# Performance work log

Measured on AMD Instinct MI355X. Metric: run time of the kernel, lower is better.

The kernel has to match this reference:

```python
import jax, jax.numpy as jnp
import numpy as np

HID = 128   # hidden_dim
NCLS = 10   # n_classes
B = 64      # number of graphs in the batched heterograph
NC, NP, NN = 100000, 400000, 150000  # component / port / net node counts
E = 400000  # edges per edge type


def setup_inputs() -> dict:
    key = jax.random.key(0)
    ks = jax.random.split(key, 32)
    f32 = jnp.float32

    def w(k, shape, fan_in):
        return jax.random.normal(k, shape, dtype=f32) * (1.0 / np.sqrt(fan_in))

    inp = {
        "h_comp": jax.random.normal(ks[0], (NC, 1), f32),
        "h_port": jax.random.normal(ks[1], (NP, 2), f32),
        "h_net": jax.random.normal(ks[2], (NN, 1), f32),
        "e_cp_src": jax.random.randint(ks[3], (E,), 0, NC, dtype=jnp.int32),
        "e_cp_dst": jax.random.randint(ks[4], (E,), 0, NP, dtype=jnp.int32),
        "e_pn_src": jax.random.randint(ks[5], (E,), 0, NP, dtype=jnp.int32),
        "e_pn_dst": jax.random.randint(ks[6], (E,), 0, NN, dtype=jnp.int32),
        "gid_comp": jnp.sort(jax.random.randint(ks[7], (NC,), 0, B, dtype=jnp.int32)),
        "gid_port": jnp.sort(jax.random.randint(ks[8], (NP,), 0, B, dtype=jnp.int32)),
        "gid_net": jnp.sort(jax.random.randint(ks[9], (NN,), 0, B, dtype=jnp.int32)),
        # GraphConv weights/biases per (layer, edge_type)
        "W1_cp": w(ks[10], (1, HID), 1), "b1_cp": jnp.zeros((HID,), f32),
        "W1_pn": w(ks[11], (2, HID), 2), "b1_pn": jnp.zeros((HID,), f32),
        "W2_cp": w(ks[12], (HID, HID), HID), "b2_cp": jnp.zeros((HID,), f32),
        "W2_pn": w(ks[13], (HID, HID), HID), "b2_pn": jnp.zeros((HID,), f32),
        "W3_cp": w(ks[14], (HID, HID), HID), "b3_cp": jnp.zeros((HID,), f32),
        "W3_pn": w(ks[15], (HID, HID), HID), "b3_pn": jnp.zeros((HID,), f32),
        # classify MLP (input dim 4 = 1+2+1 pooled original features)
        "Wc1": w(ks[16], (4, HID), 4), "bc1": jnp.zeros((HID,), f32),
        "Wc2": w(ks[17], (HID, HID), HID), "bc2": jnp.zeros((HID,), f32),
        "Wc3": w(ks[18], (HID, NCLS), HID), "bc3": jnp.zeros((NCLS,), f32),
    }
    return inp


def reference(h_comp, h_port, h_net,
              e_cp_src, e_cp_dst, e_pn_src, e_pn_dst,
              gid_comp, gid_port, gid_net,
              W1_cp, b1_cp, W1_pn, b1_pn,
              W2_cp, b2_cp, W2_pn, b2_pn,
              W3_cp, b3_cp, W3_pn, b3_pn,
              Wc1, bc1, Wc2, bc2, Wc3, bc3):
    seg = jax.ops.segment_sum

    # --- HeteroGraphConv layers (faithful to original forward, including its
    # bug: DGL HeteroGraphConv drops node types with no incoming relation, so
    # 'component' vanishes after conv1 and 'port' after conv2; conv3 runs on an
    # empty dict; conv outputs are never written back to g, hence dead code).
    # GraphConv(norm='none'): dst = sum_{edges} (x_src @ W) + b
    port1 = jax.nn.relu(seg((h_comp @ W1_cp)[e_cp_src], e_cp_dst, num_segments=NP) + b1_cp)
    net1 = jax.nn.relu(seg((h_port @ W1_pn)[e_pn_src], e_pn_dst, num_segments=NN) + b1_pn)
    net2 = jax.nn.relu(seg((port1 @ W2_pn)[e_pn_src], e_pn_dst, num_segments=NN) + b2_pn)
    # conv3: skipped entirely (no src types remain in the feature dict)
    del net1, net2  # never used by the original module's output path

    # --- dgl.mean_nodes reads g.nodes[*].data['h'] = ORIGINAL input features
    def gmean(x, gid):
        s = seg(x, gid, num_segments=B)
        c = seg(jnp.ones((x.shape[0], 1), x.dtype), gid, num_segments=B)
        return s / jnp.maximum(c, 1.0)

    hg = jnp.concatenate([gmean(h_comp, gid_comp),
                          gmean(h_port, gid_port),
                          gmean(h_net, gid_net)], axis=1)  # [B, 4]

    h = jax.nn.relu(hg @ Wc1 + bc1)
    h = jax.nn.relu(h @ Wc2 + bc2)
    return h @ Wc3 + bc3  # [B, n_classes]
```

## Files before the change

kernel.cpp:

```cpp
#include <hip/hip_runtime.h>
#include <hip/hip_bf16.h>


#define NGRAPH 64
#define NB_COMP 120
#define NB_PORT 723
#define NB_NET  181
#define NSLOT (NB_COMP + NB_PORT + NB_NET)


template <int NF>
__device__ void reduce_type(const float* __restrict__ h, const int* __restrict__ gid, int n,
                            float (*bins)[NGRAPH][4],
                            int nblocks, int bid) {
    int nv = (n + 3) >> 2;
    int per = (nv + nblocks - 1) / nblocks;
    int start = bid * per;
    int end = min(nv, start + per);
    int set = threadIdx.x & 3;

    int cur = -1;
    float s0 = 0.f, s1 = 0.f, cnt = 0.f;

    for (int iv = start + (int)threadIdx.x; iv < end; iv += (int)blockDim.x) {
        int i = iv * 4;
        int g[4];
        float v0[4], v1[4];
        if (i + 3 < n) {
            int4 g4 = ((const int4*)gid)[iv];
            g[0] = g4.x; g[1] = g4.y; g[2] = g4.z; g[3] = g4.w;
            if (NF == 1) {
                float4 hv = ((const float4*)h)[iv];
                v0[0] = hv.x; v0[1] = hv.y; v0[2] = hv.z; v0[3] = hv.w;
            } else {
                float4 ha = ((const float4*)h)[iv * 2];
                float4 hb = ((const float4*)h)[iv * 2 + 1];
                v0[0] = ha.x; v1[0] = ha.y; v0[1] = ha.z; v1[1] = ha.w;
                v0[2] = hb.x; v1[2] = hb.y; v0[3] = hb.z; v1[3] = hb.w;
            }
        } else {
#pragma unroll
            for (int t = 0; t < 4; ++t) {
                if (i + t < n) {
                    g[t] = gid[i + t];
                    if (NF == 1) { v0[t] = h[i + t]; }
                    else { v0[t] = h[(i + t) * 2]; v1[t] = h[(i + t) * 2 + 1]; }
                } else {
                    g[t] = -2;
                    v0[t] = 0.f; v1[t] = 0.f;
                }
            }
        }
#pragma unroll
        for (int t = 0; t < 4; ++t) {
            if (g[t] == -2) continue;
            if (g[t] != cur) {
                if (cur >= 0) {
                    atomicAdd(&bins[set][cur][0], s0);
                    if (NF == 2) atomicAdd(&bins[set][cur][1], s1);
                    atomicAdd(&bins[set][cur][2], cnt);
                }
                cur = g[t]; s0 = 0.f; s1 = 0.f; cnt = 0.f;
            }
            s0 += v0[t];
            if (NF == 2) s1 += v1[t];
            cnt += 1.f;
        }
    }
    if (cur >= 0) {
        atomicAdd(&bins[set][cur][0], s0);
        if (NF == 2) atomicAdd(&bins[set][cur][1], s1);
        atomicAdd(&bins[set][cur][2], cnt);
    }
}

__global__ __launch_bounds__(256) void reduce_kernel(
    const float* __restrict__ h_comp, const float* __restrict__ h_port,
    const float* __restrict__ h_net,
    const int* __restrict__ gid_comp, const int* __restrict__ gid_port,
    const int* __restrict__ gid_net,
    int n_comp, int n_port, int n_net,
    float4* __restrict__ ws4) {
    __shared__ float bins[4][NGRAPH][4];
    int tid = threadIdx.x;
    int bid = blockIdx.x;

    for (int i = tid; i < 4 * NGRAPH * 4; i += blockDim.x) ((float*)bins)[i] = 0.f;
    __syncthreads();

    if (bid < NB_COMP) {
        reduce_type<1>(h_comp, gid_comp, n_comp, bins, NB_COMP, bid);
    } else if (bid < NB_COMP + NB_PORT) {
        reduce_type<2>(h_port, gid_port, n_port, bins, NB_PORT, bid - NB_COMP);
    } else {
        reduce_type<1>(h_net, gid_net, n_net, bins, NB_NET, bid - NB_COMP - NB_PORT);
    }
    __syncthreads();

    if (tid < NGRAPH) {
        float s0 = bins[0][tid][0] + bins[1][tid][0] + bins[2][tid][0] + bins[3][tid][0];
        float s1 = bins[0][tid][1] + bins[1][tid][1] + bins[2][tid][1] + bins[3][tid][1];
        float c  = bins[0][tid][2] + bins[1][tid][2] + bins[2][tid][2] + bins[3][tid][2];
        ws4[(size_t)tid * NSLOT + bid] = make_float4(s0, s1, c, 0.f);
    }
}

__global__ __launch_bounds__(256) void mlp_kernel(
    const float4* __restrict__ ws4,
    const float* __restrict__ Wc1, const float* __restrict__ bc1,
    const float* __restrict__ Wc2, const float* __restrict__ bc2,
    const float* __restrict__ Wc3, const float* __restrict__ bc3,
    float* __restrict__ out) {
    __shared__ float wred[4][8];
    __shared__ float hgs[4];
    __shared__ float h1[128];
    __shared__ float part[2][128];
    __shared__ float h2[128];
    __shared__ float l3[16][12];

    int g = blockIdx.x;
    int tid = threadIdx.x;

    float cs = 0.f, cc = 0.f, p0 = 0.f, p1 = 0.f, pc = 0.f, ns = 0.f, nc = 0.f;
    for (int s = tid; s < NSLOT; s += 256) {
        float4 v = ws4[(size_t)g * NSLOT + s];
        if (s < NB_COMP) { cs += v.x; cc += v.z; }
        else if (s < NB_COMP + NB_PORT) { p0 += v.x; p1 += v.y; pc += v.z; }
        else { ns += v.x; nc += v.z; }
    }
#pragma unroll
    for (int off = 32; off > 0; off >>= 1) {
        cs += __shfl_down(cs, off); cc += __shfl_down(cc, off);
        p0 += __shfl_down(p0, off); p1 += __shfl_down(p1, off);
        pc += __shfl_down(pc, off); ns += __shfl_down(ns, off);
        nc += __shfl_down(nc, off);
    }
    int wave = tid >> 6;
    if ((tid & 63) == 0) {
        wred[wave][0] = cs; wred[wave][1] = cc; wred[wave][2] = p0; wred[wave][3] = p1;
        wred[wave][4] = pc; wred[wave][5] = ns; wred[wave][6] = nc;
    }
    __syncthreads();
    if (tid == 0) {
        float t0 = wred[0][0] + wred[1][0] + wred[2][0] + wred[3][0];
        float t1 = wred[0][1] + wred[1][1] + wred[2][1] + wred[3][1];
        float t2 = wred[0][2] + wred[1][2] + wred[2][2] + wred[3][2];
        float t3 = wred[0][3] + wred[1][3] + wred[2][3] + wred[3][3];
        float t4 = wred[0][4] + wred[1][4] + wred[2][4] + wred[3][4];
        float t5 = wred[0][5] + wred[1][5] + wred[2][5] + wred[3][5];
        float t6 = wred[0][6] + wred[1][6] + wred[2][6] + wred[3][6];
        hgs[0] = t0 / fmaxf(t1, 1.f);
        hgs[1] = t2 / fmaxf(t4, 1.f);
        hgs[2] = t3 / fmaxf(t4, 1.f);
        hgs[3] = t5 / fmaxf(t6, 1.f);
    }
    __syncthreads();

    if (tid < 128) {
        float v = hgs[0] * Wc1[tid] + hgs[1] * Wc1[128 + tid] +
                  hgs[2] * Wc1[256 + tid] + hgs[3] * Wc1[384 + tid] + bc1[tid];
        h1[tid] = fmaxf(v, 0.f);
    }
    __syncthreads();

    {
        int j = tid & 127;
        int h = tid >> 7;
        float acc = 0.f;
#pragma unroll
        for (int kk = 0; kk < 64; kk += 4) {
            int k = h * 64 + kk;
            float4 hh = *(const float4*)&h1[k];
            acc += hh.x * Wc2[(k + 0) * 128 + j] + hh.y * Wc2[(k + 1) * 128 + j] +
                   hh.z * Wc2[(k + 2) * 128 + j] + hh.w * Wc2[(k + 3) * 128 + j];
        }
        part[h][j] = acc;
    }
    __syncthreads();
    if (tid < 128) h2[tid] = fmaxf(part[0][tid] + part[1][tid] + bc2[tid], 0.f);
    __syncthreads();

    if (tid < 160) {
        int c = tid % 10;
        int seg = tid / 10;
        float a = 0.f;
#pragma unroll
        for (int k = seg * 8; k < seg * 8 + 8; ++k) a += h2[k] * Wc3[k * 10 + c];
        l3[seg][c] = a;
    }
    __syncthreads();
    if (tid < 10) {
        float a = bc3[tid];
#pragma unroll
        for (int s = 0; s < 16; ++s) a += l3[s][tid];
        out[g * 10 + tid] = a;
    }
}

extern "C" void kernel_launch(void* const* d_in, const int* in_sizes, int n_in,
                              void* d_out, int out_size, void* d_ws, size_t ws_size,
                              hipStream_t stream) {
    const float* h_comp = (const float*)d_in[0];
    const float* h_port = (const float*)d_in[1];
    const float* h_net  = (const float*)d_in[2];
    const int* gid_comp = (const int*)d_in[7];
    const int* gid_port = (const int*)d_in[8];
    const int* gid_net  = (const int*)d_in[9];
    const float* Wc1 = (const float*)d_in[22];
    const float* bc1 = (const float*)d_in[23];
    const float* Wc2 = (const float*)d_in[24];
    const float* bc2 = (const float*)d_in[25];
    const float* Wc3 = (const float*)d_in[26];
    const float* bc3 = (const float*)d_in[27];

    int n_comp = in_sizes[0];
    int n_port = in_sizes[1] / 2;
    int n_net  = in_sizes[2];

    float4* ws4 = (float4*)d_ws;
    float* out = (float*)d_out;

    reduce_kernel<<<NSLOT, 256, 0, stream>>>(
        h_comp, h_port, h_net, gid_comp, gid_port, gid_net,
        n_comp, n_port, n_net, ws4);

    mlp_kernel<<<NGRAPH, 256, 0, stream>>>(ws4, Wc1, bc1, Wc2, bc2, Wc3, bc3, out);
}
```

Measured before the change: 117.7 us.

## Fuse reduce and MLP kernels into one cooperative launch with grid sync

Merges the per-graph reduction and the classifier MLP into a single cooperative kernel, separated by a grid-wide barrier, so only one launch is issued. The first 64 blocks run the MLP after the barrier. This removes the second launch and its gap. In exchange it adds grid-sync overhead, and cooperative launch requires all 1024 blocks to be co-resident. It falls back to the two-kernel path if the cooperative launch fails.

```diff
diff --git a/kernel.cpp b/kernel.cpp
--- a/kernel.cpp
+++ b/kernel.cpp
@@ -1,5 +1,8 @@
 #include <hip/hip_runtime.h>
 #include <hip/hip_bf16.h>
+#include <hip/hip_cooperative_groups.h>
+
+namespace cg = cooperative_groups;
 
 
 #define NGRAPH 64
@@ -74,6 +77,151 @@
     }
 }
 
+__device__ __forceinline__ void phase1(
+    const float* __restrict__ h_comp, const float* __restrict__ h_port,
+    const float* __restrict__ h_net,
+    const int* __restrict__ gid_comp, const int* __restrict__ gid_port,
+    const int* __restrict__ gid_net,
+    int n_comp, int n_port, int n_net,
+    float4* __restrict__ ws4, float (*bins)[NGRAPH][4]) {
+    int tid = threadIdx.x;
+    int bid = blockIdx.x;
+
+    for (int i = tid; i < 4 * NGRAPH * 4; i += 256) ((float*)bins)[i] = 0.f;
+    __syncthreads();
+
+    if (bid < NB_COMP) {
+        reduce_type<1>(h_comp, gid_comp, n_comp, bins, NB_COMP, bid);
+    } else if (bid < NB_COMP + NB_PORT) {
+        reduce_type<2>(h_port, gid_port, n_port, bins, NB_PORT, bid - NB_COMP);
+    } else {
+        reduce_type<1>(h_net, gid_net, n_net, bins, NB_NET, bid - NB_COMP - NB_PORT);
+    }
+    __syncthreads();
+
+    if (tid < NGRAPH) {
+        float s0 = bins[0][tid][0] + bins[1][tid][0] + bins[2][tid][0] + bins[3][tid][0];
+        float s1 = bins[0][tid][1] + bins[1][tid][1] + bins[2][tid][1] + bins[3][tid][1];
+        float c  = bins[0][tid][2] + bins[1][tid][2] + bins[2][tid][2] + bins[3][tid][2];
+        ws4[(size_t)tid * NSLOT + bid] = make_float4(s0, s1, c, 0.f);
+    }
+}
+
+__device__ __forceinline__ void phase2(
+    int g, const float4* __restrict__ ws4,
+    const float* __restrict__ Wc1, const float* __restrict__ bc1,
+    const float* __restrict__ Wc2, const float* __restrict__ bc2,
+    const float* __restrict__ Wc3, const float* __restrict__ bc3,
+    float* __restrict__ out,
+    float (*wred)[8], float* hgs, float* h1, float (*part)[128],
+    float* h2, float (*l3)[12]) {
+    int tid = threadIdx.x;
+
+    float cs = 0.f, cc = 0.f, p0 = 0.f, p1 = 0.f, pc = 0.f, ns = 0.f, nc = 0.f;
+    for (int s = tid; s < NSLOT; s += 256) {
+        float4 v = ws4[(size_t)g * NSLOT + s];
+        if (s < NB_COMP) { cs += v.x; cc += v.z; }
+        else if (s < NB_COMP + NB_PORT) { p0 += v.x; p1 += v.y; pc += v.z; }
+        else { ns += v.x; nc += v.z; }
+    }
+#pragma unroll
+    for (int off = 32; off > 0; off >>= 1) {
+        cs += __shfl_down(cs, off); cc += __shfl_down(cc, off);
+        p0 += __shfl_down(p0, off); p1 += __shfl_down(p1, off);
+        pc += __shfl_down(pc, off); ns += __shfl_down(ns, off);
+        nc += __shfl_down(nc, off);
+    }
+    int wave = tid >> 6;
+    if ((tid & 63) == 0) {
+        wred[wave][0] = cs; wred[wave][1] = cc; wred[wave][2] = p0; wred[wave][3] = p1;
+        wred[wave][4] = pc; wred[wave][5] = ns; wred[wave][6] = nc;
+    }
+    __syncthreads();
+    if (tid == 0) {
+        float t0 = wred[0][0] + wred[1][0] + wred[2][0] + wred[3][0];
+        float t1 = wred[0][1] + wred[1][1] + wred[2][1] + wred[3][1];
+        float t2 = wred[0][2] + wred[1][2] + wred[2][2] + wred[3][2];
+        float t3 = wred[0][3] + wred[1][3] + wred[2][3] + wred[3][3];
+        float t4 = wred[0][4] + wred[1][4] + wred[2][4] + wred[3][4];
+        float t5 = wred[0][5] + wred[1][5] + wred[2][5] + wred[3][5];
+        float t6 = wred[0][6] + wred[1][6] + wred[2][6] + wred[3][6];
+        hgs[0] = t0 / fmaxf(t1, 1.f);
+        hgs[1] = t2 / fmaxf(t4, 1.f);
+        hgs[2] = t3 / fmaxf(t4, 1.f);
+        hgs[3] = t5 / fmaxf(t6, 1.f);
+    }
+    __syncthreads();
+
+    if (tid < 128) {
+        float v = hgs[0] * Wc1[tid] + hgs[1] * Wc1[128 + tid] +
+                  hgs[2] * Wc1[256 + tid] + hgs[3] * Wc1[384 + tid] + bc1[tid];
+        h1[tid] = fmaxf(v, 0.f);
+    }
+    __syncthreads();
+
+    {
+        int j = tid & 127;
+        int h = tid >> 7;
+        float acc = 0.f;
+#pragma unroll
+        for (int kk = 0; kk < 64; kk += 4) {
+            int k = h * 64 + kk;
+            float4 hh = *(const float4*)&h1[k];
+            acc += hh.x * Wc2[(k + 0) * 128 + j] + hh.y * Wc2[(k + 1) * 128 + j] +
+                   hh.z * Wc2[(k + 2) * 128 + j] + hh.w * Wc2[(k + 3) * 128 + j];
+        }
+        part[h][j] = acc;
+    }
+    __syncthreads();
+    if (tid < 128) h2[tid] = fmaxf(part[0][tid] + part[1][tid] + bc2[tid], 0.f);
+    __syncthreads();
+
+    if (tid < 160) {
+        int c = tid % 10;
+        int seg = tid / 10;
+        float a = 0.f;
+#pragma unroll
+        for (int k = seg * 8; k < seg * 8 + 8; ++k) a += h2[k] * Wc3[k * 10 + c];
+        l3[seg][c] = a;
+    }
+    __syncthreads();
+    if (tid < 10) {
+        float a = bc3[tid];
+#pragma unroll
+        for (int s = 0; s < 16; ++s) a += l3[s][tid];
+        out[g * 10 + tid] = a;
+    }
+}
+
+__global__ __launch_bounds__(256, 4) void fused_kernel(
+    const float* __restrict__ h_comp, const float* __restrict__ h_port,
+    const float* __restrict__ h_net,
+    const int* __restrict__ gid_comp, const int* __restrict__ gid_port,
+    const int* __restrict__ gid_net,
+    int n_comp, int n_port, int n_net,
+    const float* __restrict__ Wc1, const float* __restrict__ bc1,
+    const float* __restrict__ Wc2, const float* __restrict__ bc2,
+    const float* __restrict__ Wc3, const float* __restrict__ bc3,
+    float4* __restrict__ ws4, float* __restrict__ out) {
+    __shared__ float bins[4][NGRAPH][4];
+    __shared__ float wred[4][8];
+    __shared__ float hgs[4];
+    __shared__ float h1[128];
+    __shared__ float part[2][128];
+    __shared__ float h2[128];
+    __shared__ float l3[16][12];
+
+    phase1(h_comp, h_port, h_net, gid_comp, gid_port, gid_net,
+           n_comp, n_port, n_net, ws4, bins);
+
+    cg::this_grid().sync();
+
+    if (blockIdx.x < NGRAPH) {
+        phase2(blockIdx.x, ws4, Wc1, bc1, Wc2, bc2, Wc3, bc3, out,
+               wred, hgs, h1, part, h2, l3);
+    }
+}
+
 __global__ __launch_bounds__(256) void reduce_kernel(
     const float* __restrict__ h_comp, const float* __restrict__ h_port,
     const float* __restrict__ h_net,
@@ -82,27 +230,8 @@
     int n_comp, int n_port, int n_net,
     float4* __restrict__ ws4) {
     __shared__ float bins[4][NGRAPH][4];
-    int tid = threadIdx.x;
-    int bid = blockIdx.x;
-
-    for (int i = tid; i < 4 * NGRAPH * 4; i += blockDim.x) ((float*)bins)[i] = 0.f;
-    __syncthreads();
-
-    if (bid < NB_COMP) {
-        reduce_type<1>(h_comp, gid_comp, n_comp, bins, NB_COMP, bid);
-    } else if (bid < NB_COMP + NB_PORT) {
-        reduce_type<2>(h_port, gid_port, n_port, bins, NB_PORT, bid - NB_COMP);
-    } else {
-        reduce_type<1>(h_net, gid_net, n_net, bins, NB_NET, bid - NB_COMP - NB_PORT);
-    }
-    __syncthreads();
-
-    if (tid < NGRAPH) {
-        float s0 = bins[0][tid][0] + bins[1][tid][0] + bins[2][tid][0] + bins[3][tid][0];
-        float s1 = bins[0][tid][1] + bins[1][tid][1] + bins[2][tid][1] + bins[3][tid][1];
-        float c  = bins[0][tid][2] + bins[1][tid][2] + bins[2][tid][2] + bins[3][tid][2];
-        ws4[(size_t)tid * NSLOT + bid] = make_float4(s0, s1, c, 0.f);
-    }
+    phase1(h_comp, h_port, h_net, gid_comp, gid_port, gid_net,
+           n_comp, n_port, n_net, ws4, bins);
 }
 
 __global__ __launch_bounds__(256) void mlp_kernel(
@@ -117,84 +246,8 @@
     __shared__ float part[2][128];
     __shared__ float h2[128];
     __shared__ float l3[16][12];
-
-    int g = blockIdx.x;
-    int tid = threadIdx.x;
-
-    float cs = 0.f, cc = 0.f, p0 = 0.f, p1 = 0.f, pc = 0.f, ns = 0.f, nc = 0.f;
-    for (int s = tid; s < NSLOT; s += 256) {
-        float4 v = ws4[(size_t)g * NSLOT + s];
-        if (s < NB_COMP) { cs += v.x; cc += v.z; }
-        else if (s < NB_COMP + NB_PORT) { p0 += v.x; p1 += v.y; pc += v.z; }
-        else { ns += v.x; nc += v.z; }
-    }
-#pragma unroll
-    for (int off = 32; off > 0; off >>= 1) {
-        cs += __shfl_down(cs, off); cc += __shfl_down(cc, off);
-        p0 += __shfl_down(p0, off); p1 += __shfl_down(p1, off);
-        pc += __shfl_down(pc, off); ns += __shfl_down(ns, off);
-        nc += __shfl_down(nc, off);
-    }
-    int wave = tid >> 6;
-    if ((tid & 63) == 0) {
-        wred[wave][0] = cs; wred[wave][1] = cc; wred[wave][2] = p0; wred[wave][3] = p1;
-        wred[wave][4] = pc; wred[wave][5] = ns; wred[wave][6] = nc;
-    }
-    __syncthreads();
-    if (tid == 0) {
-        float t0 = wred[0][0] + wred[1][0] + wred[2][0] + wred[3][0];
-        float t1 = wred[0][1] + wred[1][1] + wred[2][1] + wred[3][1];
-        float t2 = wred[0][2] + wred[1][2] + wred[2][2] + wred[3][2];
-        float t3 = wred[0][3] + wred[1][3] + wred[2][3] + wred[3][3];
-        float t4 = wred[0][4] + wred[1][4] + wred[2][4] + wred[3][4];
-        float t5 = wred[0][5] + wred[1][5] + wred[2][5] + wred[3][5];
-        float t6 = wred[0][6] + wred[1][6] + wred[2][6] + wred[3][6];
-        hgs[0] = t0 / fmaxf(t1, 1.f);
-        hgs[1] = t2 / fmaxf(t4, 1.f);
-        hgs[2] = t3 / fmaxf(t4, 1.f);
-        hgs[3] = t5 / fmaxf(t6, 1.f);
-    }
-    __syncthreads();
-
-    if (tid < 128) {
-        float v = hgs[0] * Wc1[tid] + hgs[1] * Wc1[128 + tid] +
-                  hgs[2] * Wc1[256 + tid] + hgs[3] * Wc1[384 + tid] + bc1[tid];
-        h1[tid] = fmaxf(v, 0.f);
-    }
-    __syncthreads();
-
-    {
-        int j = tid & 127;
-        int h = tid >> 7;
-        float acc = 0.f;
-#pragma unroll
-        for (int kk = 0; kk < 64; kk += 4) {
-            int k = h * 64 + kk;
-            float4 hh = *(const float4*)&h1[k];
-            acc += hh.x * Wc2[(k + 0) * 128 + j] + hh.y * Wc2[(k + 1) * 128 + j] +
-                   hh.z * Wc2[(k + 2) * 128 + j] + hh.w * Wc2[(k + 3) * 128 + j];
-        }
-        part[h][j] = acc;
-    }
-    __syncthreads();
-    if (tid < 128) h2[tid] = fmaxf(part[0][tid] + part[1][tid] + bc2[tid], 0.f);
-    __syncthreads();
-
-    if (tid < 160) {
-        int c = tid % 10;
-        int seg = tid / 10;
-        float a = 0.f;
-#pragma unroll
-        for (int k = seg * 8; k < seg * 8 + 8; ++k) a += h2[k] * Wc3[k * 10 + c];
-        l3[seg][c] = a;
-    }
-    __syncthreads();
-    if (tid < 10) {
-        float a = bc3[tid];
-#pragma unroll
-        for (int s = 0; s < 16; ++s) a += l3[s][tid];
-        out[g * 10 + tid] = a;
-    }
+    phase2(blockIdx.x, ws4, Wc1, bc1, Wc2, bc2, Wc3, bc3, out,
+           wred, hgs, h1, part, h2, l3);
 }
 
 extern "C" void kernel_launch(void* const* d_in, const int* in_sizes, int n_in,
@@ -220,9 +273,20 @@
     float4* ws4 = (float4*)d_ws;
     float* out = (float*)d_out;
 
-    reduce_kernel<<<NSLOT, 256, 0, stream>>>(
-        h_comp, h_port, h_net, gid_comp, gid_port, gid_net,
-        n_comp, n_port, n_net, ws4);
-
-    mlp_kernel<<<NGRAPH, 256, 0, stream>>>(ws4, Wc1, bc1, Wc2, bc2, Wc3, bc3, out);
-}
+    void* args[] = {
+        (void*)&h_comp, (void*)&h_port, (void*)&h_net,
+        (void*)&gid_comp, (void*)&gid_port, (void*)&gid_net,
+        (void*)&n_comp, (void*)&n_port, (void*)&n_net,
+        (void*)&Wc1, (void*)&bc1, (void*)&Wc2, (void*)&bc2,
+        (void*)&Wc3, (void*)&bc3, (void*)&ws4, (void*)&out,
+    };
+    hipError_t err = hipLaunchCooperativeKernel(
+        (const void*)fused_kernel, dim3(NSLOT), dim3(256), args, 0, stream);
+
+    if (err != hipSuccess) {
+        reduce_kernel<<<NSLOT, 256, 0, stream>>>(
+            h_comp, h_port, h_net, gid_comp, gid_port, gid_net,
+            n_comp, n_port, n_net, ws4);
+        mlp_kernel<<<NGRAPH, 256, 0, stream>>>(ws4, Wc1, bc1, Wc2, bc2, Wc3, bc3, out);
+    }
+}
```

Measured after the change: 213.8 us. +81.6%, slower.
